# Kernel optimization log

Hardware: AMD Instinct MI355X
Metric: run time of the kernel (lower is better)

The kernel has to match this reference:

```python
import jax, jax.numpy as jnp
import numpy as np

N, E = 10000, 320000
IN, H, C, ED = 256, 4, 64, 64
HC = H * C
EPS = 1e-5
NEG_SLOPE = 0.2


def setup_inputs() -> dict:
    key = jax.random.key(0)
    ks = jax.random.split(key, 12)
    g = lambda k, shape, fan: jax.random.normal(k, shape, jnp.float32) * (1.0 / np.sqrt(fan))
    return {
        "x": jax.random.normal(ks[0], (N, IN), jnp.float32),
        "edge_index": jax.random.randint(ks[1], (2, E), 0, N, jnp.int64),
        "edge_attr": jax.random.normal(ks[2], (E, ED), jnp.float32),
        "Wl": g(ks[3], (HC, IN), IN),   # lin_l weight (source)
        "bl": jnp.zeros((HC,), jnp.float32),
        "Wr": g(ks[4], (HC, IN), IN),   # lin_r weight (target)
        "br": jnp.zeros((HC,), jnp.float32),
        "We": g(ks[5], (HC, ED), ED),   # lin_edge weight (no bias)
        "att": g(ks[6], (H, C), C),
        "bias": jnp.zeros((HC,), jnp.float32),
        "gamma": jnp.ones((HC,), jnp.float32),
        "beta": jnp.zeros((HC,), jnp.float32),
    }


def reference(x, edge_index, edge_attr, Wl, bl, Wr, br, We, att, bias, gamma, beta):
    src, dst = edge_index[0], edge_index[1]
    # add_self_loops with fill_value='mean': loop edge_attr = mean of incoming attrs
    ones = jnp.ones((E,), jnp.float32)
    cnt = jax.ops.segment_sum(ones, dst, num_segments=N)              # [N]
    loop_attr = jax.ops.segment_sum(edge_attr, dst, num_segments=N) / jnp.maximum(cnt, 1.0)[:, None]
    node_ids = jnp.arange(N, dtype=src.dtype)
    src_f = jnp.concatenate([src, node_ids])                          # [E+N]
    dst_f = jnp.concatenate([dst, node_ids])
    ea = jnp.concatenate([edge_attr, loop_attr], axis=0)              # [E+N, ED]

    xl = (x @ Wl.T + bl).reshape(N, H, C)   # source-side projection
    xr = (x @ Wr.T + br).reshape(N, H, C)   # target-side projection
    ep = (ea @ We.T).reshape(-1, H, C)       # edge projection

    m = xl[src_f] + xr[dst_f] + ep                                    # [E+N, H, C]
    m = jnp.where(m >= 0, m, NEG_SLOPE * m)                           # leaky_relu(0.2)
    logits = jnp.einsum("ehc,hc->eh", m, att)                        # [E+N, H]

    # segment softmax over target node dst_f (every node has a self loop)
    mx = jax.ops.segment_max(logits, dst_f, num_segments=N)
    ex = jnp.exp(logits - mx[dst_f])
    den = jax.ops.segment_sum(ex, dst_f, num_segments=N)
    alpha = ex / den[dst_f]                                           # [E+N, H]

    out = jax.ops.segment_sum(xl[src_f] * alpha[:, :, None], dst_f, num_segments=N)
    h = out.reshape(N, HC) + bias

    # SiLU then LayerNorm, dropout is identity in eval
    h = h * jax.nn.sigmoid(h)
    mu = jnp.mean(h, axis=-1, keepdims=True)
    var = jnp.mean((h - mu) ** 2, axis=-1, keepdims=True)
    h = (h - mu) * jax.lax.rsqrt(var + EPS) * gamma + beta
    return h, alpha
```

## Files before the change

### kernel.cpp

```cpp
#include <hip/hip_runtime.h>

#define N_NODES 10000
#define N_EDGES 320000
#define NE_TOT  330000
#define NEG_SLOPE 0.2f
#define LN_EPS 1e-5f

#define OFF_CNT    0u
#define OFF_FILL   40000u
#define OFF_ROWPTR 80128u
#define OFF_EIDS   120320u
#define OFF_POSE   1440512u
#define OFF_XLH    4000512u
#define OFF_XRH    9120512u
#define OFF_LOG    14240512u
#define OFF_WLF    19520512u
#define OFF_WRF    19651584u
#define OFF_WEF    19782656u
#define OFF_SD     19815424u
#define OFF_EAC    21135424u
#define OFF_EPC    63375424u

typedef __bf16 bf16x8 __attribute__((ext_vector_type(8)));
typedef float  f32x4  __attribute__((ext_vector_type(4)));
typedef unsigned short us4 __attribute__((ext_vector_type(4)));

__device__ __forceinline__ float bf2f(unsigned short u) {
    union { unsigned int i; float f; } v;
    v.i = ((unsigned int)u) << 16;
    return v.f;
}
__device__ __forceinline__ float lo2f(unsigned int u) {
    union { unsigned int i; float f; } v;
    v.i = u << 16;
    return v.f;
}
__device__ __forceinline__ float hi2f(unsigned int u) {
    union { unsigned int i; float f; } v;
    v.i = u & 0xFFFF0000u;
    return v.f;
}
__device__ __forceinline__ unsigned short f2bf(float x) {
    __bf16 b = (__bf16)x;
    return __builtin_bit_cast(unsigned short, b);
}
__device__ __forceinline__ bf16x8 cvt8(const float* p) {
    float4 v0 = *reinterpret_cast<const float4*>(p);
    float4 v1 = *reinterpret_cast<const float4*>(p + 4);
    bf16x8 t;
    t[0] = (__bf16)v0.x; t[1] = (__bf16)v0.y; t[2] = (__bf16)v0.z; t[3] = (__bf16)v0.w;
    t[4] = (__bf16)v1.x; t[5] = (__bf16)v1.y; t[6] = (__bf16)v1.z; t[7] = (__bf16)v1.w;
    return t;
}

__global__ void k_count(const int* __restrict__ ei, int* __restrict__ cnt) {
    int e = blockIdx.x * blockDim.x + threadIdx.x;
    if (e < N_EDGES) atomicAdd(&cnt[ei[N_EDGES + e]], 1);
}

__global__ void k_scan(const int* __restrict__ cnt, int* __restrict__ row_ptr) {
    __shared__ int sums[1024];
    int t = threadIdx.x;
    const int CH = 10;
    int base = t * CH;
    int s = 0;
    for (int i = 0; i < CH; i++) {
        int n = base + i;
        if (n < N_NODES) s += cnt[n] + 1;
    }
    sums[t] = s;
    __syncthreads();
    for (int off = 1; off < 1024; off <<= 1) {
        int v = (t >= off) ? sums[t - off] : 0;
        __syncthreads();
        sums[t] += v;
        __syncthreads();
    }
    int run = (t == 0) ? 0 : sums[t - 1];
    for (int i = 0; i < CH; i++) {
        int n = base + i;
        if (n < N_NODES) { row_ptr[n] = run; run += cnt[n] + 1; }
    }
    if (t == 1023) row_ptr[N_NODES] = sums[1023];
}

__global__ void k_fill(const int* __restrict__ ei, const int* __restrict__ row_ptr,
                       int* __restrict__ fill, int* __restrict__ eids,
                       int* __restrict__ sdv, int* __restrict__ pose) {
    int e = blockIdx.x * blockDim.x + threadIdx.x;
    if (e >= NE_TOT) return;
    int s, d;
    if (e < N_EDGES) { s = ei[e]; d = ei[N_EDGES + e]; }
    else             { s = e - N_EDGES; d = s; }
    int pos = atomicAdd(&fill[d], 1);
    int p = row_ptr[d] + pos;
    eids[p] = e;
    sdv[p] = s | (d << 16);
    pose[e] = p;
}

__global__ void k_permute_e(const float* __restrict__ edge_attr,
                            const int* __restrict__ pose,
                            unsigned short* __restrict__ eac) {
    int idx = blockIdx.x * blockDim.x + threadIdx.x;
    if (idx >= N_EDGES * 32) return;
    int e = idx >> 5, cp = idx & 31;
    float2 v = reinterpret_cast<const float2*>(edge_attr)[(size_t)e * 32 + cp];
    int p = pose[e];
    unsigned int u = ((unsigned int)f2bf(v.x)) | (((unsigned int)f2bf(v.y)) << 16);
    reinterpret_cast<unsigned int*>(eac)[(size_t)p * 32 + cp] = u;
}

__global__ void k_self_attr(const int* __restrict__ row_ptr,
                            const int* __restrict__ pose,
                            unsigned short* __restrict__ eac) {
    int node = (blockIdx.x << 2) + (threadIdx.x >> 6);
    int lane = threadIdx.x & 63;
    int b = row_ptr[node], en = row_ptr[node + 1];
    int selfp = pose[N_EDGES + node];
    float s0 = 0.0f, s1 = 0.0f;
    int i = b;
    for (; i + 1 < en; i += 2) {
        float a0 = bf2f(eac[(size_t)(i + 0) * 64 + lane]);
        float a1 = bf2f(eac[(size_t)(i + 1) * 64 + lane]);
        s0 += (i + 0 == selfp) ? 0.0f : a0;
        s1 += (i + 1 == selfp) ? 0.0f : a1;
    }
    for (; i < en; i++) {
        float a = bf2f(eac[(size_t)i * 64 + lane]);
        s0 += (i == selfp) ? 0.0f : a;
    }
    float s = s0 + s1;
    float c = (float)(en - b - 1);
    eac[(size_t)selfp * 64 + lane] = f2bf(s / fmaxf(c, 1.0f));
}

__global__ void k_prep_wfrag(const float* __restrict__ Wl,
                             const float* __restrict__ Wr,
                             const float* __restrict__ We,
                             unsigned short* __restrict__ wlf,
                             unsigned short* __restrict__ wrf,
                             unsigned short* __restrict__ wef) {
    int idx = blockIdx.x * 256 + threadIdx.x;
    if (idx >= 8192) return;
    int ln = idx & 63;
    int ts = (idx >> 6) & 7;
    int ct = idx >> 9;
    int c = ct * 16 + (ln & 15);
    int k0 = ts * 32 + (ln >> 4) * 8;
    *reinterpret_cast<bf16x8*>(wlf + (size_t)idx * 8) = cvt8(Wl + (size_t)c * 256 + k0);
    *reinterpret_cast<bf16x8*>(wrf + (size_t)idx * 8) = cvt8(Wr + (size_t)c * 256 + k0);
    if (idx < 2048) {
        int f = idx >> 6;
        int cb = f >> 1, step = f & 1;
        int ce = cb * 16 + (ln & 15);
        int ke = step * 32 + (ln >> 4) * 8;
        *reinterpret_cast<bf16x8*>(wef + (size_t)idx * 8) = cvt8(We + (size_t)ce * 64 + ke);
    }
}

__global__ __launch_bounds__(256) void k_gemm_mfma(
        const float* __restrict__ x,
        const float* __restrict__ bl, const float* __restrict__ br,
        const unsigned short* __restrict__ wlf,
        const unsigned short* __restrict__ wrf,
        unsigned short* __restrict__ xlh,
        unsigned short* __restrict__ xrh) {
    __shared__ __bf16 xs[8 * 64 * 8];
    int tid = threadIdx.x;
    int nb = blockIdx.x * 16;

    for (int f = tid; f < 512; f += 256) {
        int t = f >> 6, ln = f & 63;
        int node = nb + (ln & 15);
        int k0 = t * 32 + (ln >> 4) * 8;
        *reinterpret_cast<bf16x8*>(&xs[f * 8]) = cvt8(x + (size_t)node * 256 + k0);
    }
    __syncthreads();

    int lane = tid & 63;
    int wv = tid >> 6;
    int quad = lane >> 4;
    int ln15 = lane & 15;

    bf16x8 bfr[8];
#pragma unroll
    for (int t = 0; t < 8; t++)
        bfr[t] = *reinterpret_cast<const bf16x8*>(&xs[(t * 64 + lane) * 8]);

    int node = nb + ln15;
#pragma unroll
    for (int ci = 0; ci < 4; ci++) {
        int ct = wv * 4 + ci;
        f32x4 accl, accr;
        accl[0] = accl[1] = accl[2] = accl[3] = 0.0f;
        accr[0] = accr[1] = accr[2] = accr[3] = 0.0f;
#pragma unroll
        for (int t = 0; t < 8; t++) {
            bf16x8 al = *reinterpret_cast<const bf16x8*>(
                wlf + ((size_t)(ct * 8 + t) * 64 + lane) * 8);
            accl = __builtin_amdgcn_mfma_f32_16x16x32_bf16(al, bfr[t], accl, 0, 0, 0);
        }
#pragma unroll
        for (int t = 0; t < 8; t++) {
            bf16x8 ar = *reinterpret_cast<const bf16x8*>(
                wrf + ((size_t)(ct * 8 + t) * 64 + lane) * 8);
            accr = __builtin_amdgcn_mfma_f32_16x16x32_bf16(ar, bfr[t], accr, 0, 0, 0);
        }
        int cbase = ct * 16 + quad * 4;
        float4 blv = *reinterpret_cast<const float4*>(bl + cbase);
        float4 brv = *reinterpret_cast<const float4*>(br + cbase);
        us4 ol, orr;
        ol[0] = f2bf(accl[0] + blv.x); ol[1] = f2bf(accl[1] + blv.y);
        ol[2] = f2bf(accl[2] + blv.z); ol[3] = f2bf(accl[3] + blv.w);
        orr[0] = f2bf(accr[0] + brv.x); orr[1] = f2bf(accr[1] + brv.y);
        orr[2] = f2bf(accr[2] + brv.z); orr[3] = f2bf(accr[3] + brv.w);
        *reinterpret_cast<us4*>(xlh + (size_t)node * 256 + cbase) = ol;
        *reinterpret_cast<us4*>(xrh + (size_t)node * 256 + cbase) = orr;
    }
}

__global__ __launch_bounds__(256) void k_ep_gemm(
        const unsigned short* __restrict__ eac,
        const unsigned short* __restrict__ wef,
        unsigned short* __restrict__ epc) {
    __shared__ __bf16 wef_s[2048 * 8];
    int tid = threadIdx.x;
    for (int f = tid; f < 2048; f += 256) {
        *reinterpret_cast<bf16x8*>(&wef_s[(size_t)f * 8]) =
            *reinterpret_cast<const bf16x8*>(wef + (size_t)f * 8);
    }
    __syncthreads();

    int lane = tid & 63;
    int wv = tid >> 6;
    int quad = lane >> 4;
    int ln15 = lane & 15;

    const int ntiles = NE_TOT / 16;
#pragma unroll 1
    for (int t = blockIdx.x * 4 + wv; t < ntiles; t += gridDim.x * 4) {
        int pos = t * 16 + ln15;
        const unsigned short* row = eac + (size_t)pos * 64;
        bf16x8 b0 = *reinterpret_cast<const bf16x8*>(row + quad * 8);
        bf16x8 b1 = *reinterpret_cast<const bf16x8*>(row + 32 + quad * 8);
        unsigned short* orow = epc + (size_t)pos * 256;
#pragma unroll
        for (int cb = 0; cb < 16; cb++) {
            f32x4 acc;
            acc[0] = acc[1] = acc[2] = acc[3] = 0.0f;
            bf16x8 a0 = *reinterpret_cast<const bf16x8*>(
                &wef_s[((size_t)(cb * 2 + 0) * 64 + lane) * 8]);
            bf16x8 a1 = *reinterpret_cast<const bf16x8*>(
                &wef_s[((size_t)(cb * 2 + 1) * 64 + lane) * 8]);
            acc = __builtin_amdgcn_mfma_f32_16x16x32_bf16(a0, b0, acc, 0, 0, 0);
            acc = __builtin_amdgcn_mfma_f32_16x16x32_bf16(a1, b1, acc, 0, 0, 0);
            us4 o;
            o[0] = f2bf(acc[0]); o[1] = f2bf(acc[1]);
            o[2] = f2bf(acc[2]); o[3] = f2bf(acc[3]);
            *reinterpret_cast<us4*>(orow + cb * 16 + quad * 4) = o;
        }
    }
}

__device__ __forceinline__ float edge_logit(uint2 xlv, uint2 epv,
        float xra, float xrb, float xrc, float xrd, float4 atv) {
    float v0 = lo2f(xlv.x) + xra + lo2f(epv.x); v0 = fmaxf(v0, NEG_SLOPE * v0);
    float v1 = hi2f(xlv.x) + xrb + hi2f(epv.x); v1 = fmaxf(v1, NEG_SLOPE * v1);
    float v2 = lo2f(xlv.y) + xrc + lo2f(epv.y); v2 = fmaxf(v2, NEG_SLOPE * v2);
    float v3 = hi2f(xlv.y) + xrd + hi2f(epv.y); v3 = fmaxf(v3, NEG_SLOPE * v3);
    float hs = fmaf(v0, atv.x, fmaf(v1, atv.y, fmaf(v2, atv.z, v3 * atv.w)));
    hs += __shfl_xor(hs, 1, 64);
    hs += __shfl_xor(hs, 2, 64);
    hs += __shfl_xor(hs, 4, 64);
    hs += __shfl_xor(hs, 8, 64);
    return hs;
}

__global__ __launch_bounds__(256) void k_node_fused(
        const int* __restrict__ sdv,
        const int* __restrict__ row_ptr,
        const int* __restrict__ eids,
        const unsigned short* __restrict__ epc,
        const unsigned short* __restrict__ xlh,
        const unsigned short* __restrict__ xrh,
        const float* __restrict__ att,
        const float* __restrict__ bias,
        const float* __restrict__ gamma,
        const float* __restrict__ beta,
        float* __restrict__ lbuf,
        float* __restrict__ hout,
        float* __restrict__ alpha_out) {
    __shared__ float lsc[4][1024];
    int tid = threadIdx.x;
    int wv = tid >> 6, lane = tid & 63;
    int node = blockIdx.x * 4 + wv;
    int h = lane >> 4, l15 = lane & 15;
    int b = row_ptr[node], en = row_ptr[node + 1];
    int len = en - b;
    bool big = len > 256;
    float* ls = lsc[wv];

    const uint2* xl2 = reinterpret_cast<const uint2*>(xlh);
    const uint2* ep2 = reinterpret_cast<const uint2*>(epc);
    float4 atv = reinterpret_cast<const float4*>(att)[lane];
    uint2 xrv = reinterpret_cast<const uint2*>(xrh)[(size_t)node * 64 + lane];
    float xra = lo2f(xrv.x), xrb = hi2f(xrv.x);
    float xrc = lo2f(xrv.y), xrd = hi2f(xrv.y);

    int i = b;
    for (; i + 1 < en; i += 2) {
        int sd0 = sdv[i], sd1 = sdv[i + 1];
        int s0 = sd0 & 0xFFFF, s1 = sd1 & 0xFFFF;
        uint2 xl0 = xl2[(size_t)s0 * 64 + lane];
        uint2 e0v = ep2[(size_t)i * 64 + lane];
        uint2 xl1 = xl2[(size_t)s1 * 64 + lane];
        uint2 e1v = ep2[(size_t)(i + 1) * 64 + lane];
        float h0 = edge_logit(xl0, e0v, xra, xrb, xrc, xrd, atv);
        float h1 = edge_logit(xl1, e1v, xra, xrb, xrc, xrd, atv);
        if (l15 == 0) {
            if (!big) {
                ls[(i - b) * 4 + h] = h0;
                ls[(i + 1 - b) * 4 + h] = h1;
            } else {
                lbuf[(size_t)i * 4 + h] = h0;
                lbuf[(size_t)(i + 1) * 4 + h] = h1;
            }
        }
    }
    if (i < en) {
        int sd0 = sdv[i];
        int s0 = sd0 & 0xFFFF;
        uint2 xl0 = xl2[(size_t)s0 * 64 + lane];
        uint2 e0v = ep2[(size_t)i * 64 + lane];
        float h0 = edge_logit(xl0, e0v, xra, xrb, xrc, xrd, atv);
        if (l15 == 0) {
            if (!big) ls[(i - b) * 4 + h] = h0;
            else      lbuf[(size_t)i * 4 + h] = h0;
        }
    }

    float mh = -INFINITY;
    for (int j = l15; j < len; j += 16) {
        float lg = big ? lbuf[(size_t)(b + j) * 4 + h] : ls[j * 4 + h];
        mh = fmaxf(mh, lg);
    }
    mh = fmaxf(mh, __shfl_xor(mh, 1, 64));
    mh = fmaxf(mh, __shfl_xor(mh, 2, 64));
    mh = fmaxf(mh, __shfl_xor(mh, 4, 64));
    mh = fmaxf(mh, __shfl_xor(mh, 8, 64));
    float den = 0.0f;
    for (int j = l15; j < len; j += 16) {
        float lg = big ? lbuf[(size_t)(b + j) * 4 + h] : ls[j * 4 + h];
        den += __expf(lg - mh);
    }
    den += __shfl_xor(den, 1, 64);
    den += __shfl_xor(den, 2, 64);
    den += __shfl_xor(den, 4, 64);
    den += __shfl_xor(den, 8, 64);
    float rden = 1.0f / den;

    float acx = 0.0f, acy = 0.0f, acz = 0.0f, acw = 0.0f;
    i = b;
    for (; i + 1 < en; i += 2) {
        int sd0 = sdv[i], sd1 = sdv[i + 1];
        int e0 = eids[i], e1 = eids[i + 1];
        int s0 = sd0 & 0xFFFF, s1 = sd1 & 0xFFFF;
        uint2 xl0 = xl2[(size_t)s0 * 64 + lane];
        uint2 xl1 = xl2[(size_t)s1 * 64 + lane];
        float lg0 = big ? lbuf[(size_t)i * 4 + h]       : ls[(i - b) * 4 + h];
        float lg1 = big ? lbuf[(size_t)(i + 1) * 4 + h] : ls[(i + 1 - b) * 4 + h];
        float a0 = __expf(lg0 - mh) * rden;
        float a1 = __expf(lg1 - mh) * rden;
        if (l15 == 0) {
            alpha_out[(size_t)e0 * 4 + h] = a0;
            alpha_out[(size_t)e1 * 4 + h] = a1;
        }
        acx = fmaf(a0, lo2f(xl0.x), acx); acy = fmaf(a0, hi2f(xl0.x), acy);
        acz = fmaf(a0, lo2f(xl0.y), acz); acw = fmaf(a0, hi2f(xl0.y), acw);
        acx = fmaf(a1, lo2f(xl1.x), acx); acy = fmaf(a1, hi2f(xl1.x), acy);
        acz = fmaf(a1, lo2f(xl1.y), acz); acw = fmaf(a1, hi2f(xl1.y), acw);
    }
    if (i < en) {
        int sd0 = sdv[i];
        int e0 = eids[i];
        int s0 = sd0 & 0xFFFF;
        uint2 xl0 = xl2[(size_t)s0 * 64 + lane];
        float lg0 = big ? lbuf[(size_t)i * 4 + h] : ls[(i - b) * 4 + h];
        float a0 = __expf(lg0 - mh) * rden;
        if (l15 == 0) alpha_out[(size_t)e0 * 4 + h] = a0;
        acx = fmaf(a0, lo2f(xl0.x), acx); acy = fmaf(a0, hi2f(xl0.x), acy);
        acz = fmaf(a0, lo2f(xl0.y), acz); acw = fmaf(a0, hi2f(xl0.y), acw);
    }

    const float4 b4 = reinterpret_cast<const float4*>(bias)[lane];
    float4 hv;
    hv.x = acx + b4.x; hv.y = acy + b4.y;
    hv.z = acz + b4.z; hv.w = acw + b4.w;
    hv.x = hv.x / (1.0f + __expf(-hv.x));
    hv.y = hv.y / (1.0f + __expf(-hv.y));
    hv.z = hv.z / (1.0f + __expf(-hv.z));
    hv.w = hv.w / (1.0f + __expf(-hv.w));
    float s1 = hv.x + hv.y + hv.z + hv.w;
    float s2 = hv.x * hv.x + hv.y * hv.y + hv.z * hv.z + hv.w * hv.w;
#pragma unroll
    for (int off = 1; off < 64; off <<= 1) {
        s1 += __shfl_xor(s1, off, 64);
        s2 += __shfl_xor(s2, off, 64);
    }
    float mu = s1 * (1.0f / 256.0f);
    float var = s2 * (1.0f / 256.0f) - mu * mu;
    float rs = rsqrtf(var + LN_EPS);
    const float4 g4 = reinterpret_cast<const float4*>(gamma)[lane];
    const float4 be4 = reinterpret_cast<const float4*>(beta)[lane];
    float4 o;
    o.x = (hv.x - mu) * rs * g4.x + be4.x;
    o.y = (hv.y - mu) * rs * g4.y + be4.y;
    o.z = (hv.z - mu) * rs * g4.z + be4.z;
    o.w = (hv.w - mu) * rs * g4.w + be4.w;
    reinterpret_cast<float4*>(hout)[node * 64 + lane] = o;
}

extern "C" void kernel_launch(void* const* d_in, const int* in_sizes, int n_in,
                              void* d_out, int out_size, void* d_ws, size_t ws_size,
                              hipStream_t stream) {
    (void)in_sizes; (void)n_in; (void)out_size; (void)ws_size;
    const float* x         = (const float*)d_in[0];
    const int*   ei        = (const int*)d_in[1];
    const float* edge_attr = (const float*)d_in[2];
    const float* Wl        = (const float*)d_in[3];
    const float* bl        = (const float*)d_in[4];
    const float* Wr        = (const float*)d_in[5];
    const float* br        = (const float*)d_in[6];
    const float* We        = (const float*)d_in[7];
    const float* att       = (const float*)d_in[8];
    const float* bias      = (const float*)d_in[9];
    const float* gamma     = (const float*)d_in[10];
    const float* beta      = (const float*)d_in[11];

    char* ws = (char*)d_ws;
    int*   cnt     = (int*)(ws + OFF_CNT);
    int*   fill    = (int*)(ws + OFF_FILL);
    int*   row_ptr = (int*)(ws + OFF_ROWPTR);
    int*   eids    = (int*)(ws + OFF_EIDS);
    int*   pose    = (int*)(ws + OFF_POSE);
    unsigned short* xlh = (unsigned short*)(ws + OFF_XLH);
    unsigned short* xrh = (unsigned short*)(ws + OFF_XRH);
    float* lbuf    = (float*)(ws + OFF_LOG);
    unsigned short* wlf = (unsigned short*)(ws + OFF_WLF);
    unsigned short* wrf = (unsigned short*)(ws + OFF_WRF);
    unsigned short* wef = (unsigned short*)(ws + OFF_WEF);
    int*   sdv     = (int*)(ws + OFF_SD);
    unsigned short* eac = (unsigned short*)(ws + OFF_EAC);
    unsigned short* epc = (unsigned short*)(ws + OFF_EPC);

    float* hout      = (float*)d_out;
    float* alpha_out = (float*)d_out + N_NODES * 256;

    hipMemsetAsync(ws + OFF_CNT, 0, 2 * N_NODES * sizeof(int), stream);

    k_count<<<(N_EDGES + 255) / 256, 256, 0, stream>>>(ei, cnt);
    k_scan<<<1, 1024, 0, stream>>>(cnt, row_ptr);
    k_prep_wfrag<<<32, 256, 0, stream>>>(Wl, Wr, We, wlf, wrf, wef);
    k_fill<<<(NE_TOT + 255) / 256, 256, 0, stream>>>(ei, row_ptr, fill, eids, sdv, pose);
    k_gemm_mfma<<<N_NODES / 16, 256, 0, stream>>>(x, bl, br, wlf, wrf, xlh, xrh);
    k_permute_e<<<(N_EDGES * 32) / 256, 256, 0, stream>>>(edge_attr, pose, eac);
    k_self_attr<<<N_NODES / 4, 256, 0, stream>>>(row_ptr, pose, eac);
    k_ep_gemm<<<1024, 256, 0, stream>>>(eac, wef, epc);
    k_node_fused<<<N_NODES / 4, 256, 0, stream>>>(sdv, row_ptr, eids, epc, xlh, xrh,
                                                  att, bias, gamma, beta, lbuf,
                                                  hout, alpha_out);
}
```

Baseline: 380.6 us.

## Fuse edge projection GEMM into node kernel with online softmax aggregation

Removes the separate edge-projection GEMM kernel and its large bf16 intermediate buffer (330k x 256). Each wave now computes the projection for groups of 16 incoming edges with MFMA into swizzled LDS, then evaluates logits. It also accumulates the softmax-weighted sum in a single online pass, so xl rows are no longer gathered twice. The trade-offs are weight fragments read from global memory on every group instead of from LDS, extra LDS use that may lower occupancy, and partially wasted MFMA work on tail groups.

```diff
diff --git a/kernel.cpp b/kernel.cpp
--- a/kernel.cpp
+++ b/kernel.cpp
@@ -19,7 +19,6 @@
 #define OFF_WEF    19782656u
 #define OFF_SD     19815424u
 #define OFF_EAC    21135424u
-#define OFF_EPC    63375424u
 
 typedef __bf16 bf16x8 __attribute__((ext_vector_type(8)));
 typedef float  f32x4  __attribute__((ext_vector_type(4)));
@@ -220,68 +219,12 @@
     }
 }
 
-__global__ __launch_bounds__(256) void k_ep_gemm(
-        const unsigned short* __restrict__ eac,
-        const unsigned short* __restrict__ wef,
-        unsigned short* __restrict__ epc) {
-    __shared__ __bf16 wef_s[2048 * 8];
-    int tid = threadIdx.x;
-    for (int f = tid; f < 2048; f += 256) {
-        *reinterpret_cast<bf16x8*>(&wef_s[(size_t)f * 8]) =
-            *reinterpret_cast<const bf16x8*>(wef + (size_t)f * 8);
-    }
-    __syncthreads();
-
-    int lane = tid & 63;
-    int wv = tid >> 6;
-    int quad = lane >> 4;
-    int ln15 = lane & 15;
-
-    const int ntiles = NE_TOT / 16;
-#pragma unroll 1
-    for (int t = blockIdx.x * 4 + wv; t < ntiles; t += gridDim.x * 4) {
-        int pos = t * 16 + ln15;
-        const unsigned short* row = eac + (size_t)pos * 64;
-        bf16x8 b0 = *reinterpret_cast<const bf16x8*>(row + quad * 8);
-        bf16x8 b1 = *reinterpret_cast<const bf16x8*>(row + 32 + quad * 8);
-        unsigned short* orow = epc + (size_t)pos * 256;
-#pragma unroll
-        for (int cb = 0; cb < 16; cb++) {
-            f32x4 acc;
-            acc[0] = acc[1] = acc[2] = acc[3] = 0.0f;
-            bf16x8 a0 = *reinterpret_cast<const bf16x8*>(
-                &wef_s[((size_t)(cb * 2 + 0) * 64 + lane) * 8]);
-            bf16x8 a1 = *reinterpret_cast<const bf16x8*>(
-                &wef_s[((size_t)(cb * 2 + 1) * 64 + lane) * 8]);
-            acc = __builtin_amdgcn_mfma_f32_16x16x32_bf16(a0, b0, acc, 0, 0, 0);
-            acc = __builtin_amdgcn_mfma_f32_16x16x32_bf16(a1, b1, acc, 0, 0, 0);
-            us4 o;
-            o[0] = f2bf(acc[0]); o[1] = f2bf(acc[1]);
-            o[2] = f2bf(acc[2]); o[3] = f2bf(acc[3]);
-            *reinterpret_cast<us4*>(orow + cb * 16 + quad * 4) = o;
-        }
-    }
-}
-
-__device__ __forceinline__ float edge_logit(uint2 xlv, uint2 epv,
-        float xra, float xrb, float xrc, float xrd, float4 atv) {
-    float v0 = lo2f(xlv.x) + xra + lo2f(epv.x); v0 = fmaxf(v0, NEG_SLOPE * v0);
-    float v1 = hi2f(xlv.x) + xrb + hi2f(epv.x); v1 = fmaxf(v1, NEG_SLOPE * v1);
-    float v2 = lo2f(xlv.y) + xrc + lo2f(epv.y); v2 = fmaxf(v2, NEG_SLOPE * v2);
-    float v3 = hi2f(xlv.y) + xrd + hi2f(epv.y); v3 = fmaxf(v3, NEG_SLOPE * v3);
-    float hs = fmaf(v0, atv.x, fmaf(v1, atv.y, fmaf(v2, atv.z, v3 * atv.w)));
-    hs += __shfl_xor(hs, 1, 64);
-    hs += __shfl_xor(hs, 2, 64);
-    hs += __shfl_xor(hs, 4, 64);
-    hs += __shfl_xor(hs, 8, 64);
-    return hs;
-}
-
 __global__ __launch_bounds__(256) void k_node_fused(
         const int* __restrict__ sdv,
         const int* __restrict__ row_ptr,
         const int* __restrict__ eids,
-        const unsigned short* __restrict__ epc,
+        const unsigned short* __restrict__ eac,
+        const unsigned short* __restrict__ wef,
         const unsigned short* __restrict__ xlh,
         const unsigned short* __restrict__ xrh,
         const float* __restrict__ att,
@@ -291,6 +234,7 @@
         float* __restrict__ lbuf,
         float* __restrict__ hout,
         float* __restrict__ alpha_out) {
+    __shared__ unsigned short ep_s[4][4096];
     __shared__ float lsc[4][1024];
     int tid = threadIdx.x;
     int wv = tid >> 6, lane = tid & 63;
@@ -300,103 +244,98 @@
     int len = en - b;
     bool big = len > 256;
     float* ls = lsc[wv];
+    unsigned short* eps = ep_s[wv];
 
     const uint2* xl2 = reinterpret_cast<const uint2*>(xlh);
-    const uint2* ep2 = reinterpret_cast<const uint2*>(epc);
     float4 atv = reinterpret_cast<const float4*>(att)[lane];
     uint2 xrv = reinterpret_cast<const uint2*>(xrh)[(size_t)node * 64 + lane];
     float xra = lo2f(xrv.x), xrb = hi2f(xrv.x);
     float xrc = lo2f(xrv.y), xrd = hi2f(xrv.y);
 
-    int i = b;
-    for (; i + 1 < en; i += 2) {
-        int sd0 = sdv[i], sd1 = sdv[i + 1];
-        int s0 = sd0 & 0xFFFF, s1 = sd1 & 0xFFFF;
-        uint2 xl0 = xl2[(size_t)s0 * 64 + lane];
-        uint2 e0v = ep2[(size_t)i * 64 + lane];
-        uint2 xl1 = xl2[(size_t)s1 * 64 + lane];
-        uint2 e1v = ep2[(size_t)(i + 1) * 64 + lane];
-        float h0 = edge_logit(xl0, e0v, xra, xrb, xrc, xrd, atv);
-        float h1 = edge_logit(xl1, e1v, xra, xrb, xrc, xrd, atv);
-        if (l15 == 0) {
-            if (!big) {
-                ls[(i - b) * 4 + h] = h0;
-                ls[(i + 1 - b) * 4 + h] = h1;
+    float m = -INFINITY, den = 0.0f;
+    float acx = 0.0f, acy = 0.0f, acz = 0.0f, acw = 0.0f;
+
+    int wswz = (l15 & 7) << 3;
+    int wbase = l15 * 256;
+
+    int ngroups = (len + 15) >> 4;
+#pragma unroll 1
+    for (int g = 0; g < ngroups; g++) {
+        int pos0 = b + g * 16;
+        int jn = en - pos0; if (jn > 16) jn = 16;
+        int jc = (l15 < jn) ? l15 : (jn - 1);
+        int sdl = sdv[pos0 + jc];
+
+        const unsigned short* row = eac + (size_t)(pos0 + jc) * 64;
+        bf16x8 b0 = *reinterpret_cast<const bf16x8*>(row + h * 8);
+        bf16x8 b1 = *reinterpret_cast<const bf16x8*>(row + 32 + h * 8);
+#pragma unroll
+        for (int cb = 0; cb < 16; cb++) {
+            f32x4 acc;
+            acc[0] = acc[1] = acc[2] = acc[3] = 0.0f;
+            bf16x8 a0 = *reinterpret_cast<const bf16x8*>(
+                wef + ((size_t)(cb * 2 + 0) * 64 + lane) * 8);
+            bf16x8 a1 = *reinterpret_cast<const bf16x8*>(
+                wef + ((size_t)(cb * 2 + 1) * 64 + lane) * 8);
+            acc = __builtin_amdgcn_mfma_f32_16x16x32_bf16(a0, b0, acc, 0, 0, 0);
+            acc = __builtin_amdgcn_mfma_f32_16x16x32_bf16(a1, b1, acc, 0, 0, 0);
+            us4 o;
+            o[0] = f2bf(acc[0]); o[1] = f2bf(acc[1]);
+            o[2] = f2bf(acc[2]); o[3] = f2bf(acc[3]);
+            *reinterpret_cast<us4*>(&eps[wbase + ((cb * 16 + h * 4) ^ wswz)]) = o;
+        }
+
+#pragma unroll 4
+        for (int j = 0; j < jn; j++) {
+            int pos = pos0 + j;
+            int s = __shfl(sdl, j, 64) & 0xFFFF;
+            uint2 xlv = xl2[(size_t)s * 64 + lane];
+            us4 epv = *reinterpret_cast<const us4*>(
+                &eps[j * 256 + ((lane * 4) ^ ((j & 7) << 3))]);
+            float v0 = lo2f(xlv.x) + xra + bf2f(epv[0]); v0 = fmaxf(v0, NEG_SLOPE * v0);
+            float v1 = hi2f(xlv.x) + xrb + bf2f(epv[1]); v1 = fmaxf(v1, NEG_SLOPE * v1);
+            float v2 = lo2f(xlv.y) + xrc + bf2f(epv[2]); v2 = fmaxf(v2, NEG_SLOPE * v2);
+            float v3 = hi2f(xlv.y) + xrd + bf2f(epv[3]); v3 = fmaxf(v3, NEG_SLOPE * v3);
+            float hs = fmaf(v0, atv.x, fmaf(v1, atv.y, fmaf(v2, atv.z, v3 * atv.w)));
+            hs += __shfl_xor(hs, 1, 64);
+            hs += __shfl_xor(hs, 2, 64);
+            hs += __shfl_xor(hs, 4, 64);
+            hs += __shfl_xor(hs, 8, 64);
+            if (l15 == 0) {
+                if (!big) ls[(pos - b) * 4 + h] = hs;
+                else      lbuf[(size_t)pos * 4 + h] = hs;
+            }
+            if (hs <= m) {
+                float p = __expf(hs - m);
+                den += p;
+                acx = fmaf(p, lo2f(xlv.x), acx);
+                acy = fmaf(p, hi2f(xlv.x), acy);
+                acz = fmaf(p, lo2f(xlv.y), acz);
+                acw = fmaf(p, hi2f(xlv.y), acw);
             } else {
-                lbuf[(size_t)i * 4 + h] = h0;
-                lbuf[(size_t)(i + 1) * 4 + h] = h1;
+                float r = __expf(m - hs);
+                den = fmaf(den, r, 1.0f);
+                acx = fmaf(acx, r, lo2f(xlv.x));
+                acy = fmaf(acy, r, hi2f(xlv.x));
+                acz = fmaf(acz, r, lo2f(xlv.y));
+                acw = fmaf(acw, r, hi2f(xlv.y));
+                m = hs;
             }
         }
     }
-    if (i < en) {
-        int sd0 = sdv[i];
-        int s0 = sd0 & 0xFFFF;
-        uint2 xl0 = xl2[(size_t)s0 * 64 + lane];
-        uint2 e0v = ep2[(size_t)i * 64 + lane];
-        float h0 = edge_logit(xl0, e0v, xra, xrb, xrc, xrd, atv);
-        if (l15 == 0) {
-            if (!big) ls[(i - b) * 4 + h] = h0;
-            else      lbuf[(size_t)i * 4 + h] = h0;
-        }
-    }
-
-    float mh = -INFINITY;
+    float rden = 1.0f / den;
+
     for (int j = l15; j < len; j += 16) {
         float lg = big ? lbuf[(size_t)(b + j) * 4 + h] : ls[j * 4 + h];
-        mh = fmaxf(mh, lg);
-    }
-    mh = fmaxf(mh, __shfl_xor(mh, 1, 64));
-    mh = fmaxf(mh, __shfl_xor(mh, 2, 64));
-    mh = fmaxf(mh, __shfl_xor(mh, 4, 64));
-    mh = fmaxf(mh, __shfl_xor(mh, 8, 64));
-    float den = 0.0f;
-    for (int j = l15; j < len; j += 16) {
-        float lg = big ? lbuf[(size_t)(b + j) * 4 + h] : ls[j * 4 + h];
-        den += __expf(lg - mh);
-    }
-    den += __shfl_xor(den, 1, 64);
-    den += __shfl_xor(den, 2, 64);
-    den += __shfl_xor(den, 4, 64);
-    den += __shfl_xor(den, 8, 64);
-    float rden = 1.0f / den;
-
-    float acx = 0.0f, acy = 0.0f, acz = 0.0f, acw = 0.0f;
-    i = b;
-    for (; i + 1 < en; i += 2) {
-        int sd0 = sdv[i], sd1 = sdv[i + 1];
-        int e0 = eids[i], e1 = eids[i + 1];
-        int s0 = sd0 & 0xFFFF, s1 = sd1 & 0xFFFF;
-        uint2 xl0 = xl2[(size_t)s0 * 64 + lane];
-        uint2 xl1 = xl2[(size_t)s1 * 64 + lane];
-        float lg0 = big ? lbuf[(size_t)i * 4 + h]       : ls[(i - b) * 4 + h];
-        float lg1 = big ? lbuf[(size_t)(i + 1) * 4 + h] : ls[(i + 1 - b) * 4 + h];
-        float a0 = __expf(lg0 - mh) * rden;
-        float a1 = __expf(lg1 - mh) * rden;
-        if (l15 == 0) {
-            alpha_out[(size_t)e0 * 4 + h] = a0;
-            alpha_out[(size_t)e1 * 4 + h] = a1;
-        }
-        acx = fmaf(a0, lo2f(xl0.x), acx); acy = fmaf(a0, hi2f(xl0.x), acy);
-        acz = fmaf(a0, lo2f(xl0.y), acz); acw = fmaf(a0, hi2f(xl0.y), acw);
-        acx = fmaf(a1, lo2f(xl1.x), acx); acy = fmaf(a1, hi2f(xl1.x), acy);
-        acz = fmaf(a1, lo2f(xl1.y), acz); acw = fmaf(a1, hi2f(xl1.y), acw);
-    }
-    if (i < en) {
-        int sd0 = sdv[i];
-        int e0 = eids[i];
-        int s0 = sd0 & 0xFFFF;
-        uint2 xl0 = xl2[(size_t)s0 * 64 + lane];
-        float lg0 = big ? lbuf[(size_t)i * 4 + h] : ls[(i - b) * 4 + h];
-        float a0 = __expf(lg0 - mh) * rden;
-        if (l15 == 0) alpha_out[(size_t)e0 * 4 + h] = a0;
-        acx = fmaf(a0, lo2f(xl0.x), acx); acy = fmaf(a0, hi2f(xl0.x), acy);
-        acz = fmaf(a0, lo2f(xl0.y), acz); acw = fmaf(a0, hi2f(xl0.y), acw);
+        float a = __expf(lg - m) * rden;
+        int e = eids[b + j];
+        alpha_out[(size_t)e * 4 + h] = a;
     }
 
     const float4 b4 = reinterpret_cast<const float4*>(bias)[lane];
     float4 hv;
-    hv.x = acx + b4.x; hv.y = acy + b4.y;
-    hv.z = acz + b4.z; hv.w = acw + b4.w;
+    hv.x = acx * rden + b4.x; hv.y = acy * rden + b4.y;
+    hv.z = acz * rden + b4.z; hv.w = acw * rden + b4.w;
     hv.x = hv.x / (1.0f + __expf(-hv.x));
     hv.y = hv.y / (1.0f + __expf(-hv.y));
     hv.z = hv.z / (1.0f + __expf(-hv.z));
@@ -452,7 +391,6 @@
     unsigned short* wef = (unsigned short*)(ws + OFF_WEF);
     int*   sdv     = (int*)(ws + OFF_SD);
     unsigned short* eac = (unsigned short*)(ws + OFF_EAC);
-    unsigned short* epc = (unsigned short*)(ws + OFF_EPC);
 
     float* hout      = (float*)d_out;
     float* alpha_out = (float*)d_out + N_NODES * 256;
@@ -466,8 +404,7 @@
     k_gemm_mfma<<<N_NODES / 16, 256, 0, stream>>>(x, bl, br, wlf, wrf, xlh, xrh);
     k_permute_e<<<(N_EDGES * 32) / 256, 256, 0, stream>>>(edge_attr, pose, eac);
     k_self_attr<<<N_NODES / 4, 256, 0, stream>>>(row_ptr, pose, eac);
-    k_ep_gemm<<<1024, 256, 0, stream>>>(eac, wef, epc);
-    k_node_fused<<<N_NODES / 4, 256, 0, stream>>>(sdv, row_ptr, eids, epc, xlh, xrh,
-                                                  att, bias, gamma, beta, lbuf,
-                                                  hout, alpha_out);
-}
+    k_node_fused<<<N_NODES / 4, 256, 0, stream>>>(sdv, row_ptr, eids, eac, wef,
+                                                  xlh, xrh, att, bias, gamma, beta,
+                                                  lbuf, hout, alpha_out);
+}
```

Measured after the change: 398.8 us. +4.8%, slower.
